# Performance work log

Measured on AMD Instinct MI355X. Metric: run time of the kernel, lower is better.

Reference implementation:

```python
import jax, jax.numpy as jnp
import numpy as np


def setup_inputs() -> dict:
    key = jax.random.key(0)
    k1, k2, k3, k4 = jax.random.split(key, 4)
    B, T, C, H = 4, 2048, 1024, 64
    x = jax.random.normal(k1, (B, T, C), dtype=jnp.float32)
    # Linear(embed_dim, head_size, bias=False) weights, stored as [C, H] for x @ W
    s = 1.0 / np.sqrt(C)
    Wq = jax.random.normal(k2, (C, H), dtype=jnp.float32) * s
    Wk = jax.random.normal(k3, (C, H), dtype=jnp.float32) * s
    Wv = jax.random.normal(k4, (C, H), dtype=jnp.float32) * s
    return {"x": x, "Wq": Wq, "Wk": Wk, "Wv": Wv}


def reference(x, Wq, Wk, Wv):
    B, T, C = x.shape
    q = x @ Wq  # [B, T, H]
    k = x @ Wk
    v = x @ Wv
    # NOTE: original scales by embed_dim**-0.5 (C), not head_size**-0.5
    scale = C ** (-0.5)
    wei = jnp.einsum("bqh,bkh->bqk", q, k) * scale  # [B, T, T]
    causal = jnp.tril(jnp.ones((T, T), dtype=bool))
    wei = jnp.where(causal, wei, -jnp.inf)
    wei = jax.nn.softmax(wei, axis=-1)
    # dropout_rate = 0 -> identity
    out = jnp.einsum("bqk,bkh->bqh", wei, v)  # [B, T, H]
    return out
```

## Files before the change

kernel.cpp:

```cpp
#include <hip/hip_runtime.h>
#include <hip/hip_bf16.h>
#include <cmath>

#define B_ 4
#define T_ 2048
#define C_ 1024
#define H_ 64
#define SCALE_ 0.03125f
#define K2_ 0.04508422003f
#define THRRAW_ 177.0f
#define NEG_ -3.0e38f

typedef __attribute__((ext_vector_type(4))) float f32x4;
typedef __attribute__((ext_vector_type(8))) short s16x8;
typedef __attribute__((ext_vector_type(4))) unsigned short u16x4;

__device__ inline unsigned short f2bf(float f) {
    union { __hip_bfloat16 h; unsigned short u; } cv;
    cv.h = __float2bfloat16(f);
    return cv.u;
}

#define LDK 72

__global__ __launch_bounds__(256) void proj_mfma(
    const float* __restrict__ x, const float* __restrict__ Wq,
    const float* __restrict__ Wk, const float* __restrict__ Wv,
    unsigned short* __restrict__ qb, unsigned short* __restrict__ kb,
    unsigned short* __restrict__ vt)
{
    __shared__ unsigned short As[64 * LDK];
    __shared__ unsigned short Bs[64 * LDK];

    const int t = threadIdx.x;
    const int lane = t & 63;
    const int w = t >> 6;
    const int blk = blockIdx.x;
    const int mat = blk % 3;
    const int row0 = (blk / 3) * 64;

    const float* W = (mat == 0) ? Wq : (mat == 1) ? Wk : Wv;

    const int wr = (w >> 1) * 32;
    const int wc = (w & 1) * 32;
    const int fr = lane & 15;
    const int ko = (lane >> 4) * 8;

    f32x4 acc[2][2];
    #pragma unroll
    for (int mi = 0; mi < 2; ++mi)
        #pragma unroll
        for (int ni = 0; ni < 2; ++ni)
            acc[mi][ni] = (f32x4){0.f, 0.f, 0.f, 0.f};

    const int bcol = t & 63;
    const int bkg  = (t >> 6) * 4;

    for (int kt = 0; kt < C_; kt += 64) {
        __syncthreads();
        #pragma unroll
        for (int i = 0; i < 4; ++i) {
            int idx = t + i * 256;
            int r = idx >> 4, kc = (idx & 15) * 4;
            f32x4 xv = *(const f32x4*)(x + (size_t)(row0 + r) * C_ + kt + kc);
            u16x4 bv;
            bv.x = f2bf(xv.x); bv.y = f2bf(xv.y); bv.z = f2bf(xv.z); bv.w = f2bf(xv.w);
            *(u16x4*)&As[r * LDK + kc] = bv;
        }
        #pragma unroll
        for (int i = 0; i < 4; ++i) {
            int kk0 = bkg + i * 16;
            u16x4 bv;
            bv.x = f2bf(W[(size_t)(kt + kk0 + 0) * H_ + bcol]);
            bv.y = f2bf(W[(size_t)(kt + kk0 + 1) * H_ + bcol]);
            bv.z = f2bf(W[(size_t)(kt + kk0 + 2) * H_ + bcol]);
            bv.w = f2bf(W[(size_t)(kt + kk0 + 3) * H_ + bcol]);
            *(u16x4*)&Bs[bcol * LDK + kk0] = bv;
        }
        __syncthreads();
        #pragma unroll
        for (int ks = 0; ks < 2; ++ks) {
            s16x8 a0 = *(const s16x8*)&As[(wr + fr) * LDK + ks * 32 + ko];
            s16x8 a1 = *(const s16x8*)&As[(wr + 16 + fr) * LDK + ks * 32 + ko];
            s16x8 b0 = *(const s16x8*)&Bs[(wc + fr) * LDK + ks * 32 + ko];
            s16x8 b1 = *(const s16x8*)&Bs[(wc + 16 + fr) * LDK + ks * 32 + ko];
            acc[0][0] = __builtin_amdgcn_mfma_f32_16x16x32_bf16(a0, b0, acc[0][0], 0, 0, 0);
            acc[0][1] = __builtin_amdgcn_mfma_f32_16x16x32_bf16(a0, b1, acc[0][1], 0, 0, 0);
            acc[1][0] = __builtin_amdgcn_mfma_f32_16x16x32_bf16(a1, b0, acc[1][0], 0, 0, 0);
            acc[1][1] = __builtin_amdgcn_mfma_f32_16x16x32_bf16(a1, b1, acc[1][1], 0, 0, 0);
        }
    }

    if (mat < 2) {
        unsigned short* outb = (mat == 0) ? qb : kb;
        #pragma unroll
        for (int mi = 0; mi < 2; ++mi)
            #pragma unroll
            for (int ni = 0; ni < 2; ++ni)
                #pragma unroll
                for (int j = 0; j < 4; ++j) {
                    int row = row0 + wr + mi * 16 + (lane >> 4) * 4 + j;
                    int col = wc + ni * 16 + fr;
                    outb[(size_t)row * H_ + col] = f2bf(acc[mi][ni][j]);
                }
    } else {
        __syncthreads();
        #pragma unroll
        for (int mi = 0; mi < 2; ++mi)
            #pragma unroll
            for (int ni = 0; ni < 2; ++ni)
                #pragma unroll
                for (int j = 0; j < 4; ++j) {
                    int r = wr + mi * 16 + (lane >> 4) * 4 + j;
                    int cc = wc + ni * 16 + fr;
                    As[cc * LDK + r] = f2bf(acc[mi][ni][j]);
                }
        __syncthreads();
        int h = t >> 2, c0 = (t & 3) * 16;
        int bb = row0 >> 11, trow = row0 & 2047;
        s16x8 v0 = *(const s16x8*)&As[h * LDK + c0];
        s16x8 v1 = *(const s16x8*)&As[h * LDK + c0 + 8];
        size_t dst = (size_t)bb * H_ * T_ + (size_t)h * T_ + trow + c0;
        *(s16x8*)&vt[dst] = v0;
        *(s16x8*)&vt[dst + 8] = v1;
    }
}

__global__ __launch_bounds__(512, 4) void attn_mfma(
    const unsigned short* __restrict__ qb, const unsigned short* __restrict__ kb,
    const unsigned short* __restrict__ vt, float* __restrict__ out)
{
    __shared__ alignas(16) unsigned short Ps[8][1024];
    __shared__ float Os[8][16][68];
    __shared__ float Mm[8][16];
    __shared__ float Ll[8][16];

    const int t = threadIdx.x, lane = t & 63, w = t >> 6;
    const int fr = lane & 15, hi4 = lane >> 4;
    const int blk = blockIdx.x;
    const int b = blk & 3;
    const int qt = 127 - (blk >> 2);
    const int qbase = qt * 16;

    const unsigned short* qp = qb + ((size_t)b * T_ + qbase) * H_;
    const unsigned short* kp = kb + (size_t)b * T_ * H_;
    const unsigned short* vp = vt + (size_t)b * H_ * T_;

    s16x8 qf0 = *(const s16x8*)&qp[fr * H_ + hi4 * 8];
    s16x8 qf1 = *(const s16x8*)&qp[fr * H_ + 32 + hi4 * 8];

    const int nt = (qbase + 79) >> 6;
    const int per = (nt + 7) >> 3;
    const int tb = w * per;
    int te = tb + per; if (te > nt) te = nt;

    float m = NEG_, l = 0.f;
    f32x4 o[4];
    #pragma unroll
    for (int hf = 0; hf < 4; ++hf) o[hf] = (f32x4){0.f, 0.f, 0.f, 0.f};

    unsigned short* P = &Ps[w][0];
    const int swz = (fr & 3) << 4;
    const int qrow = qbase + fr;

    for (int kt = tb; kt < te; ++kt) {
        const int kt0 = kt << 6;

        f32x4 s[4];
        #pragma unroll
        for (int n = 0; n < 4; ++n) {
            const unsigned short* kr = &kp[(size_t)(kt0 + n * 16 + fr) * H_ + hi4 * 8];
            s16x8 kf0 = *(const s16x8*)kr;
            s16x8 kf1 = *(const s16x8*)(kr + 32);
            f32x4 a = (f32x4){0.f, 0.f, 0.f, 0.f};
            a = __builtin_amdgcn_mfma_f32_16x16x32_bf16(kf0, qf0, a, 0, 0, 0);
            a = __builtin_amdgcn_mfma_f32_16x16x32_bf16(kf1, qf1, a, 0, 0, 0);
            s[n] = a;
        }

        s16x8 vf[4][2];
        #pragma unroll
        for (int hf = 0; hf < 4; ++hf) {
            const unsigned short* vr = &vp[(size_t)(hf * 16 + fr) * T_ + kt0 + hi4 * 8];
            vf[hf][0] = *(const s16x8*)vr;
            vf[hf][1] = *(const s16x8*)(vr + 32);
        }

        if (kt0 + 63 > qbase) {
            #pragma unroll
            for (int n = 0; n < 4; ++n)
                #pragma unroll
                for (int j = 0; j < 4; ++j) {
                    int key = kt0 + n * 16 + hi4 * 4 + j;
                    s[n][j] = (key > qrow) ? NEG_ : s[n][j];
                }
        }

        float mxl = fmaxf(fmaxf(fmaxf(fmaxf(s[0][0], s[0][1]), fmaxf(s[0][2], s[0][3])),
                                fmaxf(fmaxf(s[1][0], s[1][1]), fmaxf(s[1][2], s[1][3]))),
                          fmaxf(fmaxf(fmaxf(s[2][0], s[2][1]), fmaxf(s[2][2], s[2][3])),
                                fmaxf(fmaxf(s[3][0], s[3][1]), fmaxf(s[3][2], s[3][3]))));
        if (!__all(mxl - m <= THRRAW_)) {
            float mx = fmaxf(mxl, __shfl_xor(mxl, 16));
            mx = fmaxf(mx, __shfl_xor(mx, 32));
            float mn = fmaxf(m, mx);
            float corr = exp2f((m - mn) * K2_);
            m = mn;
            l *= corr;
            #pragma unroll
            for (int j = 0; j < 4; ++j) {
                float cj = __shfl(corr, (lane & 48) + hi4 * 4 + j);
                o[0][j] *= cj; o[1][j] *= cj; o[2][j] *= cj; o[3][j] *= cj;
            }
        }
        const float nmk = -m * K2_;
        float sum = 0.f;
        #pragma unroll
        for (int n = 0; n < 4; ++n)
            #pragma unroll
            for (int j = 0; j < 4; ++j) {
                float p = exp2f(fmaf(s[n][j], K2_, nmk));
                s[n][j] = p; sum += p;
            }
        sum += __shfl_xor(sum, 16);
        sum += __shfl_xor(sum, 32);
        l += sum;

        #pragma unroll
        for (int n = 0; n < 4; ++n) {
            u16x4 pk;
            pk.x = f2bf(s[n][0]); pk.y = f2bf(s[n][1]);
            pk.z = f2bf(s[n][2]); pk.w = f2bf(s[n][3]);
            *(u16x4*)&P[fr * 64 + ((n * 16 + hi4 * 4) ^ swz)] = pk;
        }
        s16x8 pa0 = *(const s16x8*)&P[fr * 64 + ((hi4 * 8) ^ swz)];
        s16x8 pa1 = *(const s16x8*)&P[fr * 64 + ((32 + hi4 * 8) ^ swz)];

        #pragma unroll
        for (int hf = 0; hf < 4; ++hf) {
            o[hf] = __builtin_amdgcn_mfma_f32_16x16x32_bf16(pa0, vf[hf][0], o[hf], 0, 0, 0);
            o[hf] = __builtin_amdgcn_mfma_f32_16x16x32_bf16(pa1, vf[hf][1], o[hf], 0, 0, 0);
        }
    }

    if (hi4 == 0) { Mm[w][fr] = m; Ll[w][fr] = l; }
    #pragma unroll
    for (int hf = 0; hf < 4; ++hf)
        #pragma unroll
        for (int j = 0; j < 4; ++j)
            Os[w][hi4 * 4 + j][hf * 16 + fr] = o[hf][j];
    __syncthreads();

    if (t < 256) {
        int qq = t >> 4, h0 = (t & 15) * 4;
        float M = NEG_;
        #pragma unroll
        for (int s8 = 0; s8 < 8; ++s8) M = fmaxf(M, Mm[s8][qq]);
        float L = 0.f;
        f32x4 r = (f32x4){0.f, 0.f, 0.f, 0.f};
        #pragma unroll
        for (int s8 = 0; s8 < 8; ++s8) {
            float e = exp2f((Mm[s8][qq] - M) * K2_);
            L += Ll[s8][qq] * e;
            f32x4 osv = *(const f32x4*)&Os[s8][qq][h0];
            r.x = fmaf(osv.x, e, r.x);
            r.y = fmaf(osv.y, e, r.y);
            r.z = fmaf(osv.z, e, r.z);
            r.w = fmaf(osv.w, e, r.w);
        }
        float il = 1.0f / L;
        r.x *= il; r.y *= il; r.z *= il; r.w *= il;
        *(f32x4*)&out[((size_t)b * T_ + qbase + qq) * H_ + h0] = r;
    }
}

extern "C" void kernel_launch(void* const* d_in, const int* in_sizes, int n_in,
                              void* d_out, int out_size, void* d_ws, size_t ws_size,
                              hipStream_t stream) {
    const float* x  = (const float*)d_in[0];
    const float* Wq = (const float*)d_in[1];
    const float* Wk = (const float*)d_in[2];
    const float* Wv = (const float*)d_in[3];
    float* outp = (float*)d_out;

    unsigned short* base = (unsigned short*)d_ws;
    unsigned short* qbw = base;
    unsigned short* kbw = base + 524288;
    unsigned short* vtw = base + 1048576;

    proj_mfma<<<(B_ * T_ / 64) * 3, 256, 0, stream>>>(x, Wq, Wk, Wv, qbw, kbw, vtw);
    attn_mfma<<<B_ * (T_ / 16), 512, 0, stream>>>(qbw, kbw, vtw, outp);
}
```

Baseline: 48.51 us.

## Fuse QKV projection into one kernel with pre-transposed bf16 weights

Adds a small kernel that converts and transposes Wq/Wk/Wv into a single bf16 [192, C] buffer in workspace. The projection kernel is then restructured so each block handles 16 rows of x and computes all three Q/K/V outputs, reading x once instead of three times. Weight fragments are loaded directly from global/L2 instead of being staged through shared memory. This trades an extra kernel launch and more global weight loads per block for a third of the x traffic and less per-iteration conversion work.

```diff
diff --git a/kernel.cpp b/kernel.cpp
--- a/kernel.cpp
+++ b/kernel.cpp
@@ -21,108 +21,86 @@
     return cv.u;
 }
 
-#define LDK 72
-
-__global__ __launch_bounds__(256) void proj_mfma(
-    const float* __restrict__ x, const float* __restrict__ Wq,
-    const float* __restrict__ Wk, const float* __restrict__ Wv,
+__global__ __launch_bounds__(256) void wprep(
+    const float* __restrict__ Wq, const float* __restrict__ Wk,
+    const float* __restrict__ Wv, unsigned short* __restrict__ wt)
+{
+    const int g = blockIdx.x * 256 + threadIdx.x;
+    const int c = g >> 7;
+    const int kg = (g & 127) * 8;
+    const float* W = (c < 64) ? Wq : (c < 128) ? Wk : Wv;
+    const int col = c & 63;
+    u16x4 a, b;
+    a.x = f2bf(W[(size_t)(kg + 0) * H_ + col]);
+    a.y = f2bf(W[(size_t)(kg + 1) * H_ + col]);
+    a.z = f2bf(W[(size_t)(kg + 2) * H_ + col]);
+    a.w = f2bf(W[(size_t)(kg + 3) * H_ + col]);
+    b.x = f2bf(W[(size_t)(kg + 4) * H_ + col]);
+    b.y = f2bf(W[(size_t)(kg + 5) * H_ + col]);
+    b.z = f2bf(W[(size_t)(kg + 6) * H_ + col]);
+    b.w = f2bf(W[(size_t)(kg + 7) * H_ + col]);
+    *(u16x4*)&wt[(size_t)c * C_ + kg] = a;
+    *(u16x4*)&wt[(size_t)c * C_ + kg + 4] = b;
+}
+
+__global__ __launch_bounds__(256) void proj_fused(
+    const float* __restrict__ x, const unsigned short* __restrict__ wt,
     unsigned short* __restrict__ qb, unsigned short* __restrict__ kb,
     unsigned short* __restrict__ vt)
 {
-    __shared__ unsigned short As[64 * LDK];
-    __shared__ unsigned short Bs[64 * LDK];
-
-    const int t = threadIdx.x;
-    const int lane = t & 63;
-    const int w = t >> 6;
-    const int blk = blockIdx.x;
-    const int mat = blk % 3;
-    const int row0 = (blk / 3) * 64;
-
-    const float* W = (mat == 0) ? Wq : (mat == 1) ? Wk : Wv;
-
-    const int wr = (w >> 1) * 32;
-    const int wc = (w & 1) * 32;
-    const int fr = lane & 15;
-    const int ko = (lane >> 4) * 8;
-
-    f32x4 acc[2][2];
-    #pragma unroll
-    for (int mi = 0; mi < 2; ++mi)
-        #pragma unroll
-        for (int ni = 0; ni < 2; ++ni)
-            acc[mi][ni] = (f32x4){0.f, 0.f, 0.f, 0.f};
-
-    const int bcol = t & 63;
-    const int bkg  = (t >> 6) * 4;
+    __shared__ alignas(16) unsigned short Sh[2560];
+
+    const int t = threadIdx.x, lane = t & 63, w = t >> 6;
+    const int fr = lane & 15, hi4 = lane >> 4, ko = hi4 * 8;
+    const int row0 = blockIdx.x * 16;
+    const int wc = w * 48;
+    const int ar = t >> 4, akc = (t & 15) * 4;
+
+    f32x4 acc[3];
+    #pragma unroll
+    for (int n = 0; n < 3; ++n) acc[n] = (f32x4){0.f, 0.f, 0.f, 0.f};
 
     for (int kt = 0; kt < C_; kt += 64) {
         __syncthreads();
-        #pragma unroll
-        for (int i = 0; i < 4; ++i) {
-            int idx = t + i * 256;
-            int r = idx >> 4, kc = (idx & 15) * 4;
-            f32x4 xv = *(const f32x4*)(x + (size_t)(row0 + r) * C_ + kt + kc);
-            u16x4 bv;
-            bv.x = f2bf(xv.x); bv.y = f2bf(xv.y); bv.z = f2bf(xv.z); bv.w = f2bf(xv.w);
-            *(u16x4*)&As[r * LDK + kc] = bv;
-        }
-        #pragma unroll
-        for (int i = 0; i < 4; ++i) {
-            int kk0 = bkg + i * 16;
-            u16x4 bv;
-            bv.x = f2bf(W[(size_t)(kt + kk0 + 0) * H_ + bcol]);
-            bv.y = f2bf(W[(size_t)(kt + kk0 + 1) * H_ + bcol]);
-            bv.z = f2bf(W[(size_t)(kt + kk0 + 2) * H_ + bcol]);
-            bv.w = f2bf(W[(size_t)(kt + kk0 + 3) * H_ + bcol]);
-            *(u16x4*)&Bs[bcol * LDK + kk0] = bv;
-        }
+        f32x4 xv = *(const f32x4*)(x + (size_t)(row0 + ar) * C_ + kt + akc);
+        u16x4 bv;
+        bv.x = f2bf(xv.x); bv.y = f2bf(xv.y); bv.z = f2bf(xv.z); bv.w = f2bf(xv.w);
+        *(u16x4*)&Sh[ar * 72 + akc] = bv;
         __syncthreads();
         #pragma unroll
         for (int ks = 0; ks < 2; ++ks) {
-            s16x8 a0 = *(const s16x8*)&As[(wr + fr) * LDK + ks * 32 + ko];
-            s16x8 a1 = *(const s16x8*)&As[(wr + 16 + fr) * LDK + ks * 32 + ko];
-            s16x8 b0 = *(const s16x8*)&Bs[(wc + fr) * LDK + ks * 32 + ko];
-            s16x8 b1 = *(const s16x8*)&Bs[(wc + 16 + fr) * LDK + ks * 32 + ko];
-            acc[0][0] = __builtin_amdgcn_mfma_f32_16x16x32_bf16(a0, b0, acc[0][0], 0, 0, 0);
-            acc[0][1] = __builtin_amdgcn_mfma_f32_16x16x32_bf16(a0, b1, acc[0][1], 0, 0, 0);
-            acc[1][0] = __builtin_amdgcn_mfma_f32_16x16x32_bf16(a1, b0, acc[1][0], 0, 0, 0);
-            acc[1][1] = __builtin_amdgcn_mfma_f32_16x16x32_bf16(a1, b1, acc[1][1], 0, 0, 0);
-        }
-    }
-
-    if (mat < 2) {
-        unsigned short* outb = (mat == 0) ? qb : kb;
-        #pragma unroll
-        for (int mi = 0; mi < 2; ++mi)
-            #pragma unroll
-            for (int ni = 0; ni < 2; ++ni)
-                #pragma unroll
-                for (int j = 0; j < 4; ++j) {
-                    int row = row0 + wr + mi * 16 + (lane >> 4) * 4 + j;
-                    int col = wc + ni * 16 + fr;
-                    outb[(size_t)row * H_ + col] = f2bf(acc[mi][ni][j]);
-                }
-    } else {
-        __syncthreads();
-        #pragma unroll
-        for (int mi = 0; mi < 2; ++mi)
-            #pragma unroll
-            for (int ni = 0; ni < 2; ++ni)
-                #pragma unroll
-                for (int j = 0; j < 4; ++j) {
-                    int r = wr + mi * 16 + (lane >> 4) * 4 + j;
-                    int cc = wc + ni * 16 + fr;
-                    As[cc * LDK + r] = f2bf(acc[mi][ni][j]);
-                }
-        __syncthreads();
-        int h = t >> 2, c0 = (t & 3) * 16;
-        int bb = row0 >> 11, trow = row0 & 2047;
-        s16x8 v0 = *(const s16x8*)&As[h * LDK + c0];
-        s16x8 v1 = *(const s16x8*)&As[h * LDK + c0 + 8];
-        size_t dst = (size_t)bb * H_ * T_ + (size_t)h * T_ + trow + c0;
-        *(s16x8*)&vt[dst] = v0;
-        *(s16x8*)&vt[dst + 8] = v1;
+            s16x8 af = *(const s16x8*)&Sh[fr * 72 + ks * 32 + ko];
+            #pragma unroll
+            for (int n = 0; n < 3; ++n) {
+                s16x8 bf = *(const s16x8*)&wt[(size_t)(wc + n * 16 + fr) * C_ + kt + ks * 32 + ko];
+                acc[n] = __builtin_amdgcn_mfma_f32_16x16x32_bf16(af, bf, acc[n], 0, 0, 0);
+            }
+        }
+    }
+
+    const int bb = row0 >> 11, trow = row0 & 2047;
+    __syncthreads();
+    #pragma unroll
+    for (int n = 0; n < 3; ++n) {
+        int c = wc + n * 16 + fr;
+        if (c < 128) {
+            unsigned short* outb = (c < 64) ? qb : kb;
+            int cc = c & 63;
+            #pragma unroll
+            for (int j = 0; j < 4; ++j)
+                outb[(size_t)(row0 + hi4 * 4 + j) * H_ + cc] = f2bf(acc[n][j]);
+        } else {
+            int h = c - 128;
+            #pragma unroll
+            for (int j = 0; j < 4; ++j)
+                Sh[h * 20 + hi4 * 4 + j] = f2bf(acc[n][j]);
+        }
+    }
+    __syncthreads();
+    {
+        int h = t >> 2, tg = (t & 3) * 4;
+        u16x4 vv = *(const u16x4*)&Sh[h * 20 + tg];
+        *(u16x4*)&vt[(size_t)bb * (H_ * T_) + (size_t)h * T_ + trow + tg] = vv;
     }
 }
 
@@ -287,7 +265,9 @@
     unsigned short* qbw = base;
     unsigned short* kbw = base + 524288;
     unsigned short* vtw = base + 1048576;
-
-    proj_mfma<<<(B_ * T_ / 64) * 3, 256, 0, stream>>>(x, Wq, Wk, Wv, qbw, kbw, vtw);
+    unsigned short* wtw = base + 1572864;
+
+    wprep<<<96, 256, 0, stream>>>(Wq, Wk, Wv, wtw);
+    proj_fused<<<B_ * T_ / 16, 256, 0, stream>>>(x, wtw, qbw, kbw, vtw);
     attn_mfma<<<B_ * (T_ / 16), 512, 0, stream>>>(qbw, kbw, vtw, outp);
 }
```

New measurement: 69.73 us. 1.44x slower.

## Pretranspose weights to bf16 and double-buffer projection GEMM loads

Applied to the files above, without the earlier changes.

Adds a small kernel that converts Wq/Wk/Wv to bf16 and transposes them into a [3*64, C] layout in workspace. The projection kernel then loads the weights with 16-byte vector loads instead of strided scalar fp32 loads. It also double-buffers the LDS tiles, prefetching the next x/W tile into registers during the MFMAs, so there is one barrier per k-step instead of two. This costs an extra kernel launch and more LDS per block.

```diff
diff --git a/kernel.cpp b/kernel.cpp
--- a/kernel.cpp
+++ b/kernel.cpp
@@ -6,7 +6,6 @@
 #define T_ 2048
 #define C_ 1024
 #define H_ 64
-#define SCALE_ 0.03125f
 #define K2_ 0.04508422003f
 #define THRRAW_ 177.0f
 #define NEG_ -3.0e38f
@@ -14,6 +13,7 @@
 typedef __attribute__((ext_vector_type(4))) float f32x4;
 typedef __attribute__((ext_vector_type(8))) short s16x8;
 typedef __attribute__((ext_vector_type(4))) unsigned short u16x4;
+typedef __attribute__((ext_vector_type(8))) unsigned short u16x8;
 
 __device__ inline unsigned short f2bf(float f) {
     union { __hip_bfloat16 h; unsigned short u; } cv;
@@ -23,28 +23,66 @@
 
 #define LDK 72
 
-__global__ __launch_bounds__(256) void proj_mfma(
-    const float* __restrict__ x, const float* __restrict__ Wq,
-    const float* __restrict__ Wk, const float* __restrict__ Wv,
+__global__ __launch_bounds__(256) void wprep(
+    const float* __restrict__ Wq, const float* __restrict__ Wk,
+    const float* __restrict__ Wv, unsigned short* __restrict__ wt)
+{
+    const int g = blockIdx.x * 256 + threadIdx.x;
+    const int c = g >> 7;
+    const int kg = (g & 127) * 8;
+    const float* W = (c < 64) ? Wq : (c < 128) ? Wk : Wv;
+    const int col = c & 63;
+    u16x4 a, b;
+    a.x = f2bf(W[(size_t)(kg + 0) * H_ + col]);
+    a.y = f2bf(W[(size_t)(kg + 1) * H_ + col]);
+    a.z = f2bf(W[(size_t)(kg + 2) * H_ + col]);
+    a.w = f2bf(W[(size_t)(kg + 3) * H_ + col]);
+    b.x = f2bf(W[(size_t)(kg + 4) * H_ + col]);
+    b.y = f2bf(W[(size_t)(kg + 5) * H_ + col]);
+    b.z = f2bf(W[(size_t)(kg + 6) * H_ + col]);
+    b.w = f2bf(W[(size_t)(kg + 7) * H_ + col]);
+    *(u16x4*)&wt[(size_t)c * C_ + kg] = a;
+    *(u16x4*)&wt[(size_t)c * C_ + kg + 4] = b;
+}
+
+__global__ __launch_bounds__(256, 4) void proj_dbuf(
+    const float* __restrict__ x, const unsigned short* __restrict__ wt,
     unsigned short* __restrict__ qb, unsigned short* __restrict__ kb,
     unsigned short* __restrict__ vt)
 {
-    __shared__ unsigned short As[64 * LDK];
-    __shared__ unsigned short Bs[64 * LDK];
-
-    const int t = threadIdx.x;
-    const int lane = t & 63;
-    const int w = t >> 6;
+    __shared__ alignas(16) unsigned short As[2][64 * LDK];
+    __shared__ alignas(16) unsigned short Bs[2][64 * LDK];
+
+    const int t = threadIdx.x, lane = t & 63, w = t >> 6;
     const int blk = blockIdx.x;
     const int mat = blk % 3;
     const int row0 = (blk / 3) * 64;
-
-    const float* W = (mat == 0) ? Wq : (mat == 1) ? Wk : Wv;
-
-    const int wr = (w >> 1) * 32;
-    const int wc = (w & 1) * 32;
-    const int fr = lane & 15;
-    const int ko = (lane >> 4) * 8;
+    const int wr = (w >> 1) * 32, wc = (w & 1) * 32;
+    const int fr = lane & 15, ko = (lane >> 4) * 8;
+
+    const int ar0 = t >> 4, akc = (t & 15) * 4;
+    const int bc0 = t >> 3, bkc = (t & 7) * 8;
+
+    const float* xp = x + (size_t)(row0 + ar0) * C_ + akc;
+    const unsigned short* wp = wt + (size_t)(mat * 64 + bc0) * C_ + bkc;
+
+    f32x4 pa[4];
+    u16x8 pb[2];
+
+    #pragma unroll
+    for (int i = 0; i < 4; ++i) pa[i] = *(const f32x4*)(xp + (size_t)i * 16 * C_);
+    #pragma unroll
+    for (int i = 0; i < 2; ++i) pb[i] = *(const u16x8*)(wp + (size_t)i * 32 * C_);
+    #pragma unroll
+    for (int i = 0; i < 4; ++i) {
+        u16x4 bv;
+        bv.x = f2bf(pa[i].x); bv.y = f2bf(pa[i].y);
+        bv.z = f2bf(pa[i].z); bv.w = f2bf(pa[i].w);
+        *(u16x4*)&As[0][(ar0 + i * 16) * LDK + akc] = bv;
+    }
+    #pragma unroll
+    for (int i = 0; i < 2; ++i)
+        *(u16x8*)&Bs[0][(bc0 + i * 32) * LDK + bkc] = pb[i];
 
     f32x4 acc[2][2];
     #pragma unroll
@@ -53,41 +91,42 @@
         for (int ni = 0; ni < 2; ++ni)
             acc[mi][ni] = (f32x4){0.f, 0.f, 0.f, 0.f};
 
-    const int bcol = t & 63;
-    const int bkg  = (t >> 6) * 4;
-
-    for (int kt = 0; kt < C_; kt += 64) {
+    for (int it = 0; it < 16; ++it) {
         __syncthreads();
-        #pragma unroll
-        for (int i = 0; i < 4; ++i) {
-            int idx = t + i * 256;
-            int r = idx >> 4, kc = (idx & 15) * 4;
-            f32x4 xv = *(const f32x4*)(x + (size_t)(row0 + r) * C_ + kt + kc);
-            u16x4 bv;
-            bv.x = f2bf(xv.x); bv.y = f2bf(xv.y); bv.z = f2bf(xv.z); bv.w = f2bf(xv.w);
-            *(u16x4*)&As[r * LDK + kc] = bv;
-        }
-        #pragma unroll
-        for (int i = 0; i < 4; ++i) {
-            int kk0 = bkg + i * 16;
-            u16x4 bv;
-            bv.x = f2bf(W[(size_t)(kt + kk0 + 0) * H_ + bcol]);
-            bv.y = f2bf(W[(size_t)(kt + kk0 + 1) * H_ + bcol]);
-            bv.z = f2bf(W[(size_t)(kt + kk0 + 2) * H_ + bcol]);
-            bv.w = f2bf(W[(size_t)(kt + kk0 + 3) * H_ + bcol]);
-            *(u16x4*)&Bs[bcol * LDK + kk0] = bv;
-        }
-        __syncthreads();
+        const int cur = it & 1;
+        if (it < 15) {
+            const float* xn = xp + (it + 1) * 64;
+            const unsigned short* wn = wp + (it + 1) * 64;
+            #pragma unroll
+            for (int i = 0; i < 4; ++i) pa[i] = *(const f32x4*)(xn + (size_t)i * 16 * C_);
+            #pragma unroll
+            for (int i = 0; i < 2; ++i) pb[i] = *(const u16x8*)(wn + (size_t)i * 32 * C_);
+        }
+        const unsigned short* A = &As[cur][0];
+        const unsigned short* Bb = &Bs[cur][0];
         #pragma unroll
         for (int ks = 0; ks < 2; ++ks) {
-            s16x8 a0 = *(const s16x8*)&As[(wr + fr) * LDK + ks * 32 + ko];
-            s16x8 a1 = *(const s16x8*)&As[(wr + 16 + fr) * LDK + ks * 32 + ko];
-            s16x8 b0 = *(const s16x8*)&Bs[(wc + fr) * LDK + ks * 32 + ko];
-            s16x8 b1 = *(const s16x8*)&Bs[(wc + 16 + fr) * LDK + ks * 32 + ko];
+            s16x8 a0 = *(const s16x8*)&A[(wr + fr) * LDK + ks * 32 + ko];
+            s16x8 a1 = *(const s16x8*)&A[(wr + 16 + fr) * LDK + ks * 32 + ko];
+            s16x8 b0 = *(const s16x8*)&Bb[(wc + fr) * LDK + ks * 32 + ko];
+            s16x8 b1 = *(const s16x8*)&Bb[(wc + 16 + fr) * LDK + ks * 32 + ko];
             acc[0][0] = __builtin_amdgcn_mfma_f32_16x16x32_bf16(a0, b0, acc[0][0], 0, 0, 0);
             acc[0][1] = __builtin_amdgcn_mfma_f32_16x16x32_bf16(a0, b1, acc[0][1], 0, 0, 0);
             acc[1][0] = __builtin_amdgcn_mfma_f32_16x16x32_bf16(a1, b0, acc[1][0], 0, 0, 0);
             acc[1][1] = __builtin_amdgcn_mfma_f32_16x16x32_bf16(a1, b1, acc[1][1], 0, 0, 0);
+        }
+        if (it < 15) {
+            const int nxt = cur ^ 1;
+            #pragma unroll
+            for (int i = 0; i < 4; ++i) {
+                u16x4 bv;
+                bv.x = f2bf(pa[i].x); bv.y = f2bf(pa[i].y);
+                bv.z = f2bf(pa[i].z); bv.w = f2bf(pa[i].w);
+                *(u16x4*)&As[nxt][(ar0 + i * 16) * LDK + akc] = bv;
+            }
+            #pragma unroll
+            for (int i = 0; i < 2; ++i)
+                *(u16x8*)&Bs[nxt][(bc0 + i * 32) * LDK + bkc] = pb[i];
         }
     }
 
@@ -105,6 +144,7 @@
                 }
     } else {
         __syncthreads();
+        unsigned short* Tr = &As[0][0];
         #pragma unroll
         for (int mi = 0; mi < 2; ++mi)
             #pragma unroll
@@ -113,13 +153,13 @@
                 for (int j = 0; j < 4; ++j) {
                     int r = wr + mi * 16 + (lane >> 4) * 4 + j;
                     int cc = wc + ni * 16 + fr;
-                    As[cc * LDK + r] = f2bf(acc[mi][ni][j]);
+                    Tr[cc * LDK + r] = f2bf(acc[mi][ni][j]);
                 }
         __syncthreads();
         int h = t >> 2, c0 = (t & 3) * 16;
         int bb = row0 >> 11, trow = row0 & 2047;
-        s16x8 v0 = *(const s16x8*)&As[h * LDK + c0];
-        s16x8 v1 = *(const s16x8*)&As[h * LDK + c0 + 8];
+        s16x8 v0 = *(const s16x8*)&Tr[h * LDK + c0];
+        s16x8 v1 = *(const s16x8*)&Tr[h * LDK + c0 + 8];
         size_t dst = (size_t)bb * H_ * T_ + (size_t)h * T_ + trow + c0;
         *(s16x8*)&vt[dst] = v0;
         *(s16x8*)&vt[dst + 8] = v1;
@@ -287,7 +327,9 @@
     unsigned short* qbw = base;
     unsigned short* kbw = base + 524288;
     unsigned short* vtw = base + 1048576;
-
-    proj_mfma<<<(B_ * T_ / 64) * 3, 256, 0, stream>>>(x, Wq, Wk, Wv, qbw, kbw, vtw);
+    unsigned short* wtw = base + 1572864;
+
+    wprep<<<96, 256, 0, stream>>>(Wq, Wk, Wv, wtw);
+    proj_dbuf<<<(B_ * T_ / 64) * 3, 256, 0, stream>>>(x, wtw, qbw, kbw, vtw);
     attn_mfma<<<B_ * (T_ / 16), 512, 0, stream>>>(qbw, kbw, vtw, outp);
 }
```

Measured after the change: 50.20 us. 3.5% more time.
